# Optimization experiments

Hardware: AMD Instinct MI355X
Metric: run time of the kernel (lower is better)

The kernel has to match this reference:

```python
import jax, jax.numpy as jnp
import numpy as np

ROUTINGS = 3
EPS = 1e-9

def squash(s, axis=-1):
    s2 = jnp.sum(s * s, axis=axis, keepdims=True)
    scale = s2 / (1.0 + s2 + EPS)
    return scale * s / jnp.sqrt(s2 + EPS)

def setup_inputs() -> dict:
    key = jax.random.key(0)
    k1, k2 = jax.random.split(key)
    B, N_in, D_in = 64, 2048, 16
    N_out, D_out = 32, 32
    x = jax.random.normal(k1, (B, N_in, D_in), dtype=jnp.float32)
    # glorot-uniform-ish init for W [1, N_in, N_out, D_out, D_in]
    limit = np.sqrt(6.0 / (D_in + D_out)).astype(np.float32)
    W = jax.random.uniform(k2, (1, N_in, N_out, D_out, D_in), dtype=jnp.float32,
                           minval=-limit, maxval=limit)
    return {"x": x, "W": W}

def reference(x, W):
    # u_hat[b,i,j,d] = sum_k W[0,i,j,d,k] * x[b,i,k]   -> [B, N_in, N_out, D_out]
    u_hat = jnp.einsum('bik,ijdk->bijd', x, W[0])
    b = jnp.zeros(u_hat.shape[:-1], dtype=u_hat.dtype)  # [B, N_in, N_out]
    v = None
    for i in range(ROUTINGS):
        c = jax.nn.softmax(b, axis=2)                     # softmax over output capsules
        s = jnp.einsum('bij,bijd->bjd', c, u_hat)         # [B, N_out, D_out]
        v = squash(s)
        if i < ROUTINGS - 1:
            b = b + jnp.einsum('bijd,bjd->bij', u_hat, v)  # agreement update
    return v
```

## Files before the change

### kernel.cpp

```cpp
#include <hip/hip_runtime.h>
#include <cstdint>
#include <cstddef>

#define B_   64
#define NI   2048
#define DI   16
#define NO   32
#define JD   1024
#define IT   16
#define NBX  (NI/IT)
#define XSTR 260
#define EPSQ 1e-9f

typedef __attribute__((ext_vector_type(8)))  short bf16x8;
typedef __attribute__((ext_vector_type(16))) float f32x16;

__device__ __forceinline__ uint32_t pack_split(float w) {
  uint32_t u = __float_as_uint(w);
  float hf = __uint_as_float(u & 0xffff0000u);
  uint32_t lo = __float_as_uint(w - hf) >> 16;
  return (u & 0xffff0000u) | lo;
}

__device__ __forceinline__ void cvt8(const float4 a, const float4 b, bf16x8& h8, bf16x8& l8) {
  float w[8] = {a.x, a.y, a.z, a.w, b.x, b.y, b.z, b.w};
  #pragma unroll
  for (int e = 0; e < 8; ++e) {
    uint32_t u = __float_as_uint(w[e]);
    float hf = __uint_as_float(u & 0xffff0000u);
    h8[e] = (short)(u >> 16);
    l8[e] = (short)(__float_as_uint(w[e] - hf) >> 16);
  }
}

__device__ __forceinline__ f32x16 zero16() {
  f32x16 z;
  #pragma unroll
  for (int r = 0; r < 16; ++r) z[r] = 0.0f;
  return z;
}

template<bool ROUTE>
__global__ __launch_bounds__(512, 2)
void caps_pass(const float* __restrict__ x, const float* __restrict__ W,
               const float* __restrict__ vin, float* __restrict__ part)
{
  __shared__ uint32_t xl[32 * XSTR];
  __shared__ float al[NO * 32];
  __shared__ float cl[NO * 32];

  const int t    = threadIdx.x;
  const int wv   = t >> 6;
  const int l    = t & 63;
  const int col  = l & 31;
  const int hb   = l >> 5;
  const int p    = blockIdx.x;
  const int half = blockIdx.y;
  const int i0   = p * IT;
  const int b0   = half * 32;

  for (int idx = t; idx < 32 * 64; idx += 512) {
    const int bb = idx >> 6, c4 = idx & 63;
    const float4 xv = *reinterpret_cast<const float4*>(
        x + (size_t)(b0 + bb) * (NI * DI) + (size_t)i0 * DI + (c4 << 2));
    uint4 o;
    o.x = pack_split(xv.x); o.y = pack_split(xv.y);
    o.z = pack_split(xv.z); o.w = pack_split(xv.w);
    *reinterpret_cast<uint4*>(&xl[bb * XSTR + (c4 << 2)]) = o;
  }

  float vreg[4][16];
  if constexpr (ROUTE) {
    #pragma unroll
    for (int m = 0; m < 4; ++m)
      #pragma unroll
      for (int r = 0; r < 16; ++r) {
        const int row = (r & 3) + 8 * (r >> 2) + 4 * hb;
        vreg[m][r] = vin[(size_t)(b0 + col) * JD + wv * 128 + m * 32 + row];
      }
  }

  f32x16 sacc[4];
  #pragma unroll
  for (int m = 0; m < 4; ++m) sacc[m] = zero16();

  __syncthreads();

  if constexpr (!ROUTE) {
    for (int ii = 0; ii < IT; ++ii) {
      const uint4 q0 = *reinterpret_cast<const uint4*>(&xl[col * XSTR + (ii << 4) + (hb << 3)]);
      const uint4 q1 = *reinterpret_cast<const uint4*>(&xl[col * XSTR + (ii << 4) + (hb << 3) + 4]);
      bf16x8 xh, xo;
      const uint32_t qq[8] = {q0.x, q0.y, q0.z, q0.w, q1.x, q1.y, q1.z, q1.w};
      #pragma unroll
      for (int e = 0; e < 8; ++e) { xh[e] = (short)(qq[e] >> 16); xo[e] = (short)(qq[e] & 0xffff); }

      const float* wbase = W + (size_t)(i0 + ii) * (JD * DI) + (size_t)wv * 128 * DI;
      #pragma unroll
      for (int m = 0; m < 4; ++m) {
        const float* wt = wbase + m * 32 * DI + col * DI + (hb << 3);
        const float4 wa = *reinterpret_cast<const float4*>(wt);
        const float4 wb = *reinterpret_cast<const float4*>(wt + 4);
        bf16x8 wh, wl; cvt8(wa, wb, wh, wl);
        sacc[m] = __builtin_amdgcn_mfma_f32_32x32x16_bf16(wh, xh, sacc[m], 0, 0, 0);
        sacc[m] = __builtin_amdgcn_mfma_f32_32x32x16_bf16(wh, xo, sacc[m], 0, 0, 0);
        sacc[m] = __builtin_amdgcn_mfma_f32_32x32x16_bf16(wl, xh, sacc[m], 0, 0, 0);
      }
    }
  } else {
    #pragma unroll 1
    for (int ii = 0; ii < IT; ++ii) {
      const uint4 q0 = *reinterpret_cast<const uint4*>(&xl[col * XSTR + (ii << 4) + (hb << 3)]);
      const uint4 q1 = *reinterpret_cast<const uint4*>(&xl[col * XSTR + (ii << 4) + (hb << 3) + 4]);
      bf16x8 xh, xo;
      const uint32_t qq[8] = {q0.x, q0.y, q0.z, q0.w, q1.x, q1.y, q1.z, q1.w};
      #pragma unroll
      for (int e = 0; e < 8; ++e) { xh[e] = (short)(qq[e] >> 16); xo[e] = (short)(qq[e] & 0xffff); }

      const float* wbase = W + (size_t)(i0 + ii) * (JD * DI) + (size_t)wv * 128 * DI;
      f32x16 u[4];
      #pragma unroll
      for (int m = 0; m < 4; ++m) {
        const float* wt = wbase + m * 32 * DI + col * DI + (hb << 3);
        const float4 wa = *reinterpret_cast<const float4*>(wt);
        const float4 wb = *reinterpret_cast<const float4*>(wt + 4);
        bf16x8 wh, wl; cvt8(wa, wb, wh, wl);
        f32x16 c = zero16();
        c = __builtin_amdgcn_mfma_f32_32x32x16_bf16(wh, xh, c, 0, 0, 0);
        c = __builtin_amdgcn_mfma_f32_32x32x16_bf16(wh, xo, c, 0, 0, 0);
        c = __builtin_amdgcn_mfma_f32_32x32x16_bf16(wl, xh, c, 0, 0, 0);
        u[m] = c;
      }

      float ap[4];
      #pragma unroll
      for (int m = 0; m < 4; ++m) {
        float s = 0.f;
        #pragma unroll
        for (int r = 0; r < 16; ++r) s += u[m][r] * vreg[m][r];
        s += __shfl_xor(s, 32);
        ap[m] = s;
      }
      if (l < 32) {
        #pragma unroll
        for (int m = 0; m < 4; ++m) {
          const int j = (wv << 2) + m;
          al[(j << 5) + ((col + j) & 31)] = ap[m];
        }
      }
      __syncthreads();

      {
        const int jj = t & 31;
        #pragma unroll
        for (int rd = 0; rd < 2; ++rd) {
          const int bb = (t >> 5) + (rd << 4);
          const float av = al[(jj << 5) + ((bb + jj) & 31)];
          float mx = av;
          #pragma unroll
          for (int s = 1; s < 32; s <<= 1) mx = fmaxf(mx, __shfl_xor(mx, s, 32));
          const float e = __expf(av - mx);
          float den = e;
          #pragma unroll
          for (int s = 1; s < 32; s <<= 1) den += __shfl_xor(den, s, 32);
          cl[(jj << 5) + ((bb + jj) & 31)] = e / den;
        }
      }
      __syncthreads();

      #pragma unroll
      for (int m = 0; m < 4; ++m) {
        const int j = (wv << 2) + m;
        const float cv = cl[(j << 5) + ((col + j) & 31)];
        #pragma unroll
        for (int r = 0; r < 16; ++r) sacc[m][r] += cv * u[m][r];
      }
    }
  }

  #pragma unroll
  for (int m = 0; m < 4; ++m)
    #pragma unroll
    for (int r = 0; r < 16; ++r) {
      const int jd = (wv << 7) + (m << 5) + (r & 3) + 8 * (r >> 2) + (hb << 2);
      part[((size_t)(p * B_ + b0 + col) << 10) + jd] = sacc[m][r];
    }
}

__global__ void reduce_squash(const float* __restrict__ part, int nPart,
                              const float* __restrict__ vprev,
                              float* __restrict__ out, float scale, int addPrev)
{
  const int b  = blockIdx.x;
  const int jd = threadIdx.x;
  float s = 0.f;
  for (int p = 0; p < nPart; ++p)
    s += part[((size_t)(p * B_ + b) << 10) + jd];
  const float val = s * scale;
  float sq = val * val;
  #pragma unroll
  for (int w = 1; w < 32; w <<= 1) sq += __shfl_xor(sq, w, 32);
  const float f = sq / ((1.0f + sq + EPSQ) * sqrtf(sq + EPSQ));
  float o = f * val;
  if (addPrev) o += vprev[b * JD + jd];
  out[b * JD + jd] = o;
}

extern "C" void kernel_launch(void* const* d_in, const int* in_sizes, int n_in,
                              void* d_out, int out_size, void* d_ws, size_t ws_size,
                              hipStream_t stream) {
  const float* x = (const float*)d_in[0];
  const float* W = (const float*)d_in[1];
  float* ws  = (float*)d_ws;
  float* out = (float*)d_out;

  float* partb = ws;
  float* v0    = ws + (size_t)NBX * B_ * JD;
  float* vs    = v0 + B_ * JD;

  const dim3 grid(NBX, 2);
  caps_pass<false><<<grid, 512, 0, stream>>>(x, W, nullptr, partb);
  reduce_squash<<<B_, JD, 0, stream>>>(partb, NBX, nullptr, v0, 1.0f / 32.0f, 0);
  caps_pass<true><<<grid, 512, 0, stream>>>(x, W, v0, partb);
  reduce_squash<<<B_, JD, 0, stream>>>(partb, NBX, v0, vs, 1.0f, 1);
  caps_pass<true><<<grid, 512, 0, stream>>>(x, W, vs, partb);
  reduce_squash<<<B_, JD, 0, stream>>>(partb, NBX, nullptr, out, 1.0f, 0);
}
```

Measured before the change: 398.2 us.

## Prefetch W, drop softmax sync via max-free exp, recompute u_hat, vectorize reduce

In the routing pass, the next slice of W is prefetched into registers and the LDS buffer is double-buffered, so one of the two per-iteration barriers goes away. The softmax now skips max subtraction: each wave writes exp of its logits and then sums the denominator itself. u_hat is recomputed with MFMA instead of being held in registers, trading extra matrix work for lower register pressure. The partial stores and the reduce_squash kernel are vectorized to float4 with an 8-way unrolled accumulation; dropping the max subtraction risks overflow if the logits grow large.

```diff
diff --git a/kernel.cpp b/kernel.cpp
--- a/kernel.cpp
+++ b/kernel.cpp
@@ -46,8 +46,7 @@
                const float* __restrict__ vin, float* __restrict__ part)
 {
   __shared__ uint32_t xl[32 * XSTR];
-  __shared__ float al[NO * 32];
-  __shared__ float cl[NO * 32];
+  __shared__ float al[2][NO][32];
 
   const int t    = threadIdx.x;
   const int wv   = t >> 6;
@@ -108,7 +107,18 @@
       }
     }
   } else {
-    #pragma unroll 1
+    float4 wa[4], wb[4];
+    {
+      const float* wbase = W + (size_t)i0 * (JD * DI) + (size_t)wv * 128 * DI;
+      #pragma unroll
+      for (int m = 0; m < 4; ++m) {
+        const float* wt = wbase + m * 32 * DI + col * DI + (hb << 3);
+        wa[m] = *reinterpret_cast<const float4*>(wt);
+        wb[m] = *reinterpret_cast<const float4*>(wt + 4);
+      }
+    }
+
+    #pragma unroll 2
     for (int ii = 0; ii < IT; ++ii) {
       const uint4 q0 = *reinterpret_cast<const uint4*>(&xl[col * XSTR + (ii << 4) + (hb << 3)]);
       const uint4 q1 = *reinterpret_cast<const uint4*>(&xl[col * XSTR + (ii << 4) + (hb << 3) + 4]);
@@ -117,63 +127,55 @@
       #pragma unroll
       for (int e = 0; e < 8; ++e) { xh[e] = (short)(qq[e] >> 16); xo[e] = (short)(qq[e] & 0xffff); }
 
-      const float* wbase = W + (size_t)(i0 + ii) * (JD * DI) + (size_t)wv * 128 * DI;
-      f32x16 u[4];
-      #pragma unroll
-      for (int m = 0; m < 4; ++m) {
-        const float* wt = wbase + m * 32 * DI + col * DI + (hb << 3);
-        const float4 wa = *reinterpret_cast<const float4*>(wt);
-        const float4 wb = *reinterpret_cast<const float4*>(wt + 4);
-        bf16x8 wh, wl; cvt8(wa, wb, wh, wl);
-        f32x16 c = zero16();
-        c = __builtin_amdgcn_mfma_f32_32x32x16_bf16(wh, xh, c, 0, 0, 0);
-        c = __builtin_amdgcn_mfma_f32_32x32x16_bf16(wh, xo, c, 0, 0, 0);
-        c = __builtin_amdgcn_mfma_f32_32x32x16_bf16(wl, xh, c, 0, 0, 0);
-        u[m] = c;
-      }
-
-      float ap[4];
-      #pragma unroll
-      for (int m = 0; m < 4; ++m) {
+      bf16x8 wh[4], wl[4];
+      #pragma unroll
+      for (int m = 0; m < 4; ++m) cvt8(wa[m], wb[m], wh[m], wl[m]);
+      if (ii + 1 < IT) {
+        const float* wbase = W + (size_t)(i0 + ii + 1) * (JD * DI) + (size_t)wv * 128 * DI;
+        #pragma unroll
+        for (int m = 0; m < 4; ++m) {
+          const float* wt = wbase + m * 32 * DI + col * DI + (hb << 3);
+          wa[m] = *reinterpret_cast<const float4*>(wt);
+          wb[m] = *reinterpret_cast<const float4*>(wt + 4);
+        }
+      }
+
+      float eo[4];
+      #pragma unroll
+      for (int m = 0; m < 4; ++m) {
+        f32x16 u = zero16();
+        u = __builtin_amdgcn_mfma_f32_32x32x16_bf16(wh[m], xh, u, 0, 0, 0);
+        u = __builtin_amdgcn_mfma_f32_32x32x16_bf16(wh[m], xo, u, 0, 0, 0);
+        u = __builtin_amdgcn_mfma_f32_32x32x16_bf16(wl[m], xh, u, 0, 0, 0);
         float s = 0.f;
         #pragma unroll
-        for (int r = 0; r < 16; ++r) s += u[m][r] * vreg[m][r];
+        for (int r = 0; r < 16; ++r) s += u[r] * vreg[m][r];
         s += __shfl_xor(s, 32);
-        ap[m] = s;
+        eo[m] = __expf(s);
       }
       if (l < 32) {
         #pragma unroll
         for (int m = 0; m < 4; ++m) {
           const int j = (wv << 2) + m;
-          al[(j << 5) + ((col + j) & 31)] = ap[m];
+          al[ii & 1][j][(col + j) & 31] = eo[m];
         }
       }
       __syncthreads();
 
-      {
-        const int jj = t & 31;
-        #pragma unroll
-        for (int rd = 0; rd < 2; ++rd) {
-          const int bb = (t >> 5) + (rd << 4);
-          const float av = al[(jj << 5) + ((bb + jj) & 31)];
-          float mx = av;
-          #pragma unroll
-          for (int s = 1; s < 32; s <<= 1) mx = fmaxf(mx, __shfl_xor(mx, s, 32));
-          const float e = __expf(av - mx);
-          float den = e;
-          #pragma unroll
-          for (int s = 1; s < 32; s <<= 1) den += __shfl_xor(den, s, 32);
-          cl[(jj << 5) + ((bb + jj) & 31)] = e / den;
-        }
-      }
-      __syncthreads();
-
-      #pragma unroll
-      for (int m = 0; m < 4; ++m) {
-        const int j = (wv << 2) + m;
-        const float cv = cl[(j << 5) + ((col + j) & 31)];
-        #pragma unroll
-        for (int r = 0; r < 16; ++r) sacc[m][r] += cv * u[m][r];
+      float den = 0.f;
+      #pragma unroll
+      for (int j = 0; j < 32; ++j) den += al[ii & 1][j][(col + j) & 31];
+      const float rden = 1.0f / den;
+
+      #pragma unroll
+      for (int m = 0; m < 4; ++m) {
+        f32x16 u = zero16();
+        u = __builtin_amdgcn_mfma_f32_32x32x16_bf16(wh[m], xh, u, 0, 0, 0);
+        u = __builtin_amdgcn_mfma_f32_32x32x16_bf16(wh[m], xo, u, 0, 0, 0);
+        u = __builtin_amdgcn_mfma_f32_32x32x16_bf16(wl[m], xh, u, 0, 0, 0);
+        const float cm = eo[m] * rden;
+        #pragma unroll
+        for (int r = 0; r < 16; ++r) sacc[m][r] += cm * u[r];
       }
     }
   }
@@ -181,29 +183,50 @@
   #pragma unroll
   for (int m = 0; m < 4; ++m)
     #pragma unroll
-    for (int r = 0; r < 16; ++r) {
-      const int jd = (wv << 7) + (m << 5) + (r & 3) + 8 * (r >> 2) + (hb << 2);
-      part[((size_t)(p * B_ + b0 + col) << 10) + jd] = sacc[m][r];
-    }
-}
-
-__global__ void reduce_squash(const float* __restrict__ part, int nPart,
+    for (int g = 0; g < 4; ++g) {
+      const int jd = (wv << 7) + (m << 5) + (g << 3) + (hb << 2);
+      *reinterpret_cast<float4*>(part + (((size_t)(p * B_ + b0 + col)) << 10) + jd) =
+          make_float4(sacc[m][4 * g], sacc[m][4 * g + 1], sacc[m][4 * g + 2], sacc[m][4 * g + 3]);
+    }
+}
+
+__global__ void reduce_squash(const float* __restrict__ part,
                               const float* __restrict__ vprev,
                               float* __restrict__ out, float scale, int addPrev)
 {
-  const int b  = blockIdx.x;
-  const int jd = threadIdx.x;
-  float s = 0.f;
-  for (int p = 0; p < nPart; ++p)
-    s += part[((size_t)(p * B_ + b) << 10) + jd];
-  const float val = s * scale;
-  float sq = val * val;
-  #pragma unroll
-  for (int w = 1; w < 32; w <<= 1) sq += __shfl_xor(sq, w, 32);
+  const int b   = blockIdx.x;
+  const int jd0 = blockIdx.y * 512 + threadIdx.x * 4;
+
+  float4 acc[8];
+  #pragma unroll
+  for (int u = 0; u < 8; ++u) acc[u] = make_float4(0.f, 0.f, 0.f, 0.f);
+
+  for (int p = 0; p < NBX; p += 8) {
+    #pragma unroll
+    for (int u = 0; u < 8; ++u) {
+      const float4 v = *reinterpret_cast<const float4*>(
+          part + (((size_t)((p + u) * B_ + b)) << 10) + jd0);
+      acc[u].x += v.x; acc[u].y += v.y; acc[u].z += v.z; acc[u].w += v.w;
+    }
+  }
+  #pragma unroll
+  for (int u = 1; u < 8; ++u) {
+    acc[0].x += acc[u].x; acc[0].y += acc[u].y;
+    acc[0].z += acc[u].z; acc[0].w += acc[u].w;
+  }
+
+  float val[4] = {acc[0].x * scale, acc[0].y * scale, acc[0].z * scale, acc[0].w * scale};
+  float sq = val[0]*val[0] + val[1]*val[1] + val[2]*val[2] + val[3]*val[3];
+  #pragma unroll
+  for (int w = 1; w < 8; w <<= 1) sq += __shfl_xor(sq, w, 8);
+
   const float f = sq / ((1.0f + sq + EPSQ) * sqrtf(sq + EPSQ));
-  float o = f * val;
-  if (addPrev) o += vprev[b * JD + jd];
-  out[b * JD + jd] = o;
+  float4 o = make_float4(f * val[0], f * val[1], f * val[2], f * val[3]);
+  if (addPrev) {
+    const float4 vp = *reinterpret_cast<const float4*>(vprev + (size_t)b * JD + jd0);
+    o.x += vp.x; o.y += vp.y; o.z += vp.z; o.w += vp.w;
+  }
+  *reinterpret_cast<float4*>(out + (size_t)b * JD + jd0) = o;
 }
 
 extern "C" void kernel_launch(void* const* d_in, const int* in_sizes, int n_in,
@@ -219,10 +242,11 @@
   float* vs    = v0 + B_ * JD;
 
   const dim3 grid(NBX, 2);
+  const dim3 rgrid(B_, 2);
   caps_pass<false><<<grid, 512, 0, stream>>>(x, W, nullptr, partb);
-  reduce_squash<<<B_, JD, 0, stream>>>(partb, NBX, nullptr, v0, 1.0f / 32.0f, 0);
+  reduce_squash<<<rgrid, 128, 0, stream>>>(partb, nullptr, v0, 1.0f / 32.0f, 0);
   caps_pass<true><<<grid, 512, 0, stream>>>(x, W, v0, partb);
-  reduce_squash<<<B_, JD, 0, stream>>>(partb, NBX, v0, vs, 1.0f, 1);
+  reduce_squash<<<rgrid, 128, 0, stream>>>(partb, v0, vs, 1.0f, 1);
   caps_pass<true><<<grid, 512, 0, stream>>>(x, W, vs, partb);
-  reduce_squash<<<B_, JD, 0, stream>>>(partb, NBX, nullptr, out, 1.0f, 0);
-}
+  reduce_squash<<<rgrid, 128, 0, stream>>>(partb, nullptr, out, 1.0f, 0);
+}
```

Result: slower. 779.9 us (+95.9%).
